# Kernel tuning notes

Hardware: AMD Instinct MI355X
Metric: run time of the kernel (lower is better)

The kernel has to match this reference:

```python
import jax, jax.numpy as jnp
import numpy as np

NUM_CONST = 20
NUM_HIDDEN = 5
NUM_VAR = 3
NUM_GROUPS = 200
INPUT_SIZE = NUM_CONST + NUM_VAR * NUM_GROUPS   # 620
HIDDEN = NUM_HIDDEN * NUM_GROUPS                # 1000
SEQ = 8192


def setup_inputs() -> dict:
    key = jax.random.key(0)
    ks = jax.random.split(key, 5)
    s = 1.0 / np.sqrt(HIDDEN)  # PyTorch LSTM init range
    return {
        "input": jax.random.normal(ks[0], (1, SEQ, INPUT_SIZE), jnp.float32),
        "W_ih": jax.random.uniform(ks[1], (4 * HIDDEN, INPUT_SIZE), jnp.float32, -s, s),
        "W_hh": jax.random.uniform(ks[2], (4 * HIDDEN, HIDDEN), jnp.float32, -s, s),
        "b_ih": jax.random.uniform(ks[3], (4 * HIDDEN,), jnp.float32, -s, s),
        "b_hh": jax.random.uniform(ks[4], (4 * HIDDEN,), jnp.float32, -s, s),
        "keep_hidden": 1,
    }


def reference(input, W_ih, W_hh, b_ih, b_hh, keep_hidden):
    # Single-layer batch_first LSTM, batch=1, zero initial (h, c) (self.hx=None).
    x = input[0]                                  # (T, I)
    # Precompute input projections for all timesteps as one big GEMM.
    xg = x @ W_ih.T + (b_ih + b_hh)               # (T, 4H)

    def step(carry, g_x):
        h, c = carry
        g = g_x + h @ W_hh.T                      # (4H,)
        i, f, gc, o = jnp.split(g, 4)             # PyTorch gate order: i, f, g, o
        i = jax.nn.sigmoid(i)
        f = jax.nn.sigmoid(f)
        gc = jnp.tanh(gc)
        o = jax.nn.sigmoid(o)
        c = f * c + i * gc
        h = o * jnp.tanh(c)
        return (h, c), h

    h0 = jnp.zeros((HIDDEN,), input.dtype)
    c0 = jnp.zeros((HIDDEN,), input.dtype)
    _, ys = jax.lax.scan(step, (h0, c0), xg)      # ys: (T, H)
    return ys[None]                               # (1, T, H)
```

## Files before the change

kernel.cpp:

```cpp
#include <hip/hip_runtime.h>
#include <hip/hip_bf16.h>


#define IN_SZ   620
#define HID     1000
#define G4      4000
#define NWF     125
#define NW_LEG  50
#define EP_LEG  20

__device__ __forceinline__ float sigm(float v)      { return 1.0f / (1.0f + __expf(-v)); }
__device__ __forceinline__ float tanh_fast(float v) { return 2.0f / (1.0f + __expf(-2.0f * v)) - 1.0f; }

__device__ __forceinline__ void stxg_(float* p, float v) { *p = v; }
__device__ __forceinline__ void stxg_(__hip_bfloat16* p, float v) { *p = __float2bfloat16(v); }

template <typename XG>
__global__ __launch_bounds__(256) void xg_gemm2(
    const float* __restrict__ x,
    const float* __restrict__ Wih,
    const float* __restrict__ bih,
    const float* __restrict__ bhh,
    XG* __restrict__ xg,
    int T)
{
    constexpr int BM = 128, BN = 128, BK = 16, LDT = BM + 4;
    __shared__ float As[BK][LDT];
    __shared__ float Bs[BK][LDT];
    const int tid = threadIdx.x;
    const int tx = tid & 15, ty = tid >> 4;
    const int m0 = blockIdx.y * BM, n0 = blockIdx.x * BN;
    float acc[8][8] = {};

    for (int k0 = 0; k0 < IN_SZ; k0 += BK) {
        #pragma unroll
        for (int it = 0; it < 2; ++it) {
            const int r = (tid >> 2) + it * 64;
            const int c = (tid & 3) * 4;
            const int gk = k0 + c;
            {
                const int gm = m0 + r;
                float4 v = {0.f, 0.f, 0.f, 0.f};
                if (gm < T) {
                    if (gk + 3 < IN_SZ) {
                        v = *reinterpret_cast<const float4*>(x + (size_t)gm * IN_SZ + gk);
                    } else {
                        const float* row = x + (size_t)gm * IN_SZ;
                        v.x = (gk + 0 < IN_SZ) ? row[gk + 0] : 0.f;
                        v.y = (gk + 1 < IN_SZ) ? row[gk + 1] : 0.f;
                        v.z = (gk + 2 < IN_SZ) ? row[gk + 2] : 0.f;
                        v.w = (gk + 3 < IN_SZ) ? row[gk + 3] : 0.f;
                    }
                }
                As[c + 0][r] = v.x; As[c + 1][r] = v.y;
                As[c + 2][r] = v.z; As[c + 3][r] = v.w;
            }
            {
                const int gn = n0 + r;
                float4 v = {0.f, 0.f, 0.f, 0.f};
                if (gn < G4) {
                    if (gk + 3 < IN_SZ) {
                        v = *reinterpret_cast<const float4*>(Wih + (size_t)gn * IN_SZ + gk);
                    } else {
                        const float* row = Wih + (size_t)gn * IN_SZ;
                        v.x = (gk + 0 < IN_SZ) ? row[gk + 0] : 0.f;
                        v.y = (gk + 1 < IN_SZ) ? row[gk + 1] : 0.f;
                        v.z = (gk + 2 < IN_SZ) ? row[gk + 2] : 0.f;
                        v.w = (gk + 3 < IN_SZ) ? row[gk + 3] : 0.f;
                    }
                }
                Bs[c + 0][r] = v.x; Bs[c + 1][r] = v.y;
                Bs[c + 2][r] = v.z; Bs[c + 3][r] = v.w;
            }
        }
        __syncthreads();
        #pragma unroll
        for (int k = 0; k < BK; ++k) {
            float a[8], b[8];
            *reinterpret_cast<float4*>(&a[0]) = *reinterpret_cast<const float4*>(&As[k][ty * 8]);
            *reinterpret_cast<float4*>(&a[4]) = *reinterpret_cast<const float4*>(&As[k][ty * 8 + 4]);
            *reinterpret_cast<float4*>(&b[0]) = *reinterpret_cast<const float4*>(&Bs[k][tx * 8]);
            *reinterpret_cast<float4*>(&b[4]) = *reinterpret_cast<const float4*>(&Bs[k][tx * 8 + 4]);
            #pragma unroll
            for (int i = 0; i < 8; ++i)
                #pragma unroll
                for (int j = 0; j < 8; ++j)
                    acc[i][j] = fmaf(a[i], b[j], acc[i][j]);
        }
        __syncthreads();
    }

    float bias[8];
    #pragma unroll
    for (int j = 0; j < 8; ++j) {
        const int n = n0 + tx * 8 + j;
        bias[j] = (n < G4) ? (bih[n] + bhh[n]) : 0.f;
    }
    #pragma unroll
    for (int i = 0; i < 8; ++i) {
        const int m = m0 + ty * 8 + i;
        if (m >= T) continue;
        #pragma unroll
        for (int j = 0; j < 8; ++j) {
            const int n = n0 + tx * 8 + j;
            if (n < G4) {
                const int g = n / 1000, e = n - g * 1000;
                stxg_(&xg[(size_t)m * G4 + e * 4 + g], acc[i][j] + bias[j]);
            }
        }
    }
}

template <int MODE>
__device__ __forceinline__ float ldxg(const void* xg_v, size_t idx) {
    if (MODE == 0) return ((const float*)xg_v)[idx];
    return __bfloat162float(((const __hip_bfloat16*)xg_v)[idx]);
}

template <int MODE>
__global__ __launch_bounds__(256, 1) void lstm_fast(
    const void* __restrict__ xg_v,
    const float* __restrict__ Whh,
    float* __restrict__ out,
    unsigned* hb_u,
    int T)
{
    __shared__ __align__(16) unsigned hs[2][1024];
    __shared__ float gsum[4][4][2];

    const int w = blockIdx.x, tid = threadIdx.x;
    const int wave = tid >> 6, lane = tid & 63;
    const int i16 = lane & 15, p = lane >> 4;
    const int we0 = w * 8 + wave * 2;

    for (int i = tid; i < 2048; i += 256) ((unsigned*)hs)[i] = 0u;
    __syncthreads();

    const size_t rowA = (size_t)(p * HID + we0) * HID;
    const size_t rowB = rowA + HID;
    float4 wA[16], wB[16], hreg[16];
    #pragma unroll
    for (int m = 0; m < 15; ++m) {
        wA[m] = *reinterpret_cast<const float4*>(Whh + rowA + i16 * 4 + m * 64);
        wB[m] = *reinterpret_cast<const float4*>(Whh + rowB + i16 * 4 + m * 64);
    }
    if (i16 < 10) {
        wA[15] = *reinterpret_cast<const float4*>(Whh + rowA + 960 + i16 * 4);
        wB[15] = *reinterpret_cast<const float4*>(Whh + rowB + 960 + i16 * 4);
    } else {
        wA[15] = float4{0.f, 0.f, 0.f, 0.f};
        wB[15] = float4{0.f, 0.f, 0.f, 0.f};
    }

    const int gv_ = (lane >> 3) & 3;
    const int gp  = (lane >> 1) & 3;
    const int ge  = lane & 1;
    const int eg  = w * 8 + gv_ * 2 + ge;
    const int xoff = (gv_ * 2 + ge) * 4 + gp;
    const int shbase = (lane & ~7) | ge;
    float c_reg = 0.0f;
    float xv = 0.0f;
    if (wave == 0 && lane < 32)
        xv = ldxg<MODE>(xg_v, (size_t)w * 32 + xoff);

    const int tid2 = tid - 64;
    const int iA = tid2;
    const int iB = (tid2 < 58) ? (192 + tid2) : tid2;

    for (int t = 0;;) {
        const int rb = t & 1;

        #pragma unroll
        for (int m = 0; m < 15; ++m)
            hreg[m] = *reinterpret_cast<const float4*>(&hs[rb][i16 * 4 + m * 64]);
        hreg[15] = *reinterpret_cast<const float4*>(&hs[rb][960 + i16 * 4]);

        float a0 = 0.f, a1 = 0.f, a2 = 0.f, a3 = 0.f;
        float b0 = 0.f, b1 = 0.f, b2 = 0.f, b3 = 0.f;
        #pragma unroll
        for (int m = 0; m < 16; ++m) {
            const float4 hv = hreg[m];
            const float sA = fmaf(wA[m].x, hv.x, fmaf(wA[m].y, hv.y,
                             fmaf(wA[m].z, hv.z, wA[m].w * hv.w)));
            const float sB = fmaf(wB[m].x, hv.x, fmaf(wB[m].y, hv.y,
                             fmaf(wB[m].z, hv.z, wB[m].w * hv.w)));
            if ((m & 3) == 0)      { a0 += sA; b0 += sB; }
            else if ((m & 3) == 1) { a1 += sA; b1 += sB; }
            else if ((m & 3) == 2) { a2 += sA; b2 += sB; }
            else                   { a3 += sA; b3 += sB; }
        }
        float rA = (a0 + a1) + (a2 + a3);
        float rB = (b0 + b1) + (b2 + b3);
        rA += __shfl_xor(rA, 1); rB += __shfl_xor(rB, 1);
        rA += __shfl_xor(rA, 2); rB += __shfl_xor(rB, 2);
        rA += __shfl_xor(rA, 4); rB += __shfl_xor(rB, 4);
        rA += __shfl_xor(rA, 8); rB += __shfl_xor(rB, 8);
        if (i16 == 0) { gsum[wave][p][0] = rA; gsum[wave][p][1] = rB; }
        __syncthreads();

        if (wave == 0) {
            float xv_next = 0.0f;
            if (lane < 32 && t + 1 < T)
                xv_next = ldxg<MODE>(xg_v, (size_t)(t + 1) * G4 + w * 32 + xoff);

            const float g = gsum[gv_][gp][ge] + xv;
            const float act = (gp == 2) ? tanh_fast(g) : sigm(g);
            const float iv = __shfl(act, shbase);
            const float fv = __shfl(act, shbase + 2);
            const float g2 = __shfl(act, shbase + 4);
            const float ov = __shfl(act, shbase + 6);
            if (lane < 32 && gp == 0) {
                c_reg = fv * c_reg + iv * g2;
                const float h = ov * tanh_fast(c_reg);
                const unsigned hb = (__float_as_uint(h) & ~3u) | (unsigned)((t + 1) & 3);
                __hip_atomic_store(hb_u + rb * 1024 + eg, hb,
                                   __ATOMIC_RELAXED, __HIP_MEMORY_SCOPE_AGENT);
                out[(size_t)t * HID + eg] = h;
            }
            xv = xv_next;
        }

        if (++t >= T) break;

        if (wave > 0) {
            const unsigned want = (unsigned)t & 3u;
            const uint4* srcb =
                reinterpret_cast<const uint4*>(hb_u + ((t - 1) & 1) * 1024);
            __builtin_amdgcn_s_sleep(8);
            uint4 vA, vB;
            for (;;) {
                asm volatile("global_load_dwordx4 %0, %2, off sc0 sc1\n\t"
                             "global_load_dwordx4 %1, %3, off sc0 sc1\n\t"
                             "s_waitcnt vmcnt(0)"
                             : "=&v"(vA), "=&v"(vB)
                             : "v"(srcb + iA), "v"(srcb + iB)
                             : "memory");
                const unsigned bad =
                    ((vA.x ^ want) | (vA.y ^ want) | (vA.z ^ want) | (vA.w ^ want) |
                     (vB.x ^ want) | (vB.y ^ want) | (vB.z ^ want) | (vB.w ^ want)) & 3u;
                if (bad == 0u) break;
            }
            uint4* dst = reinterpret_cast<uint4*>(&hs[t & 1][0]);
            dst[iA] = vA;
            if (tid2 < 58) dst[iB] = vB;
        }
        __syncthreads();
    }
}

__global__ __launch_bounds__(256, 1) void lstm_seq_legacy(
    const float* __restrict__ x,
    const float* __restrict__ Wih,
    const float* __restrict__ Whh,
    const float* __restrict__ bih,
    const float* __restrict__ bhh,
    float* __restrict__ out,
    float* hbuf, unsigned* flags, int T)
{
    __shared__ __align__(16) float h_s[HID];
    __shared__ __align__(16) float x_s[IN_SZ + 4];
    __shared__ float pre[4][EP_LEG];

    const int w = blockIdx.x, tid = threadIdx.x;
    const int wave = tid >> 6, lane = tid & 63;
    const int i16 = lane & 15, p = lane >> 4;
    const int e0 = w * EP_LEG;

    for (int i = tid; i < HID; i += 256) h_s[i] = 0.0f;
    for (int i = tid; i < IN_SZ; i += 256) x_s[i] = x[i];
    __syncthreads();

    const float* wb_h = Whh + ((size_t)wave * HID + e0) * HID;
    const float* wb_x = Wih + ((size_t)wave * HID + e0) * IN_SZ;
    float c_reg = 0.0f;
    float bsum[4] = {0.f, 0.f, 0.f, 0.f};
    if (wave == 0 && lane < EP_LEG) {
        #pragma unroll
        for (int g = 0; g < 4; ++g) {
            int n = g * HID + e0 + lane;
            bsum[g] = bih[n] + bhh[n];
        }
    }

    for (int t = 0;;) {
        #pragma unroll
        for (int pass = 0; pass < EP_LEG / 4; ++pass) {
            const int e = pass * 4 + p;
            const float* wr = wb_h + (size_t)e * HID;
            float a0 = 0.f, a1 = 0.f, a2 = 0.f, a3 = 0.f;
            #pragma unroll
            for (int m = 0; m < 15; ++m) {
                const int kk = i16 * 4 + m * 64;
                const float4 wv = *reinterpret_cast<const float4*>(wr + kk);
                const float4 hv = *reinterpret_cast<const float4*>(&h_s[kk]);
                const float s = fmaf(wv.x, hv.x, fmaf(wv.y, hv.y, fmaf(wv.z, hv.z, wv.w * hv.w)));
                if ((m & 3) == 0) a0 += s; else if ((m & 3) == 1) a1 += s;
                else if ((m & 3) == 2) a2 += s; else a3 += s;
            }
            if (i16 < 10) {
                const int kk = i16 * 4 + 960;
                const float4 wv = *reinterpret_cast<const float4*>(wr + kk);
                const float4 hv = *reinterpret_cast<const float4*>(&h_s[kk]);
                a3 += fmaf(wv.x, hv.x, fmaf(wv.y, hv.y, fmaf(wv.z, hv.z, wv.w * hv.w)));
            }
            const float* wrx = wb_x + (size_t)e * IN_SZ;
            #pragma unroll
            for (int m = 0; m < 9; ++m) {
                const int kk = i16 * 4 + m * 64;
                const float4 wv = *reinterpret_cast<const float4*>(wrx + kk);
                const float4 hv = *reinterpret_cast<const float4*>(&x_s[kk]);
                const float s = fmaf(wv.x, hv.x, fmaf(wv.y, hv.y, fmaf(wv.z, hv.z, wv.w * hv.w)));
                if ((m & 3) == 0) a0 += s; else if ((m & 3) == 1) a1 += s;
                else if ((m & 3) == 2) a2 += s; else a3 += s;
            }
            if (i16 < 11) {
                const int kk = i16 * 4 + 576;
                const float4 wv = *reinterpret_cast<const float4*>(wrx + kk);
                const float4 hv = *reinterpret_cast<const float4*>(&x_s[kk]);
                a3 += fmaf(wv.x, hv.x, fmaf(wv.y, hv.y, fmaf(wv.z, hv.z, wv.w * hv.w)));
            }
            float acc = (a0 + a1) + (a2 + a3);
            acc += __shfl_xor(acc, 1);
            acc += __shfl_xor(acc, 2);
            acc += __shfl_xor(acc, 4);
            acc += __shfl_xor(acc, 8);
            if (i16 == 0) pre[wave][e] = acc;
        }
        __syncthreads();

        if (wave == 0 && lane < EP_LEG) {
            const float gi = pre[0][lane] + bsum[0];
            const float gf = pre[1][lane] + bsum[1];
            const float gg = pre[2][lane] + bsum[2];
            const float go = pre[3][lane] + bsum[3];
            const float iv = sigm(gi);
            const float fv = sigm(gf);
            const float gv = tanh_fast(gg);
            const float ov = sigm(go);
            c_reg = fv * c_reg + iv * gv;
            const float h = ov * tanh_fast(c_reg);
            out[(size_t)t * HID + e0 + lane] = h;
            __hip_atomic_store(&hbuf[(t & 1) * 1024 + e0 + lane], h,
                               __ATOMIC_RELAXED, __HIP_MEMORY_SCOPE_AGENT);
        }
        if (++t >= T) break;
        if (wave == 0 && lane == 0) {
            asm volatile("s_waitcnt vmcnt(0)" ::: "memory");
            __hip_atomic_store(&flags[w], (unsigned)t,
                               __ATOMIC_RELAXED, __HIP_MEMORY_SCOPE_AGENT);
        }
        if (wave > 0) {
            if (lane < NW_LEG) {
                while (__hip_atomic_load(&flags[lane], __ATOMIC_RELAXED,
                                         __HIP_MEMORY_SCOPE_AGENT) < (unsigned)t) {}
            }
            const int rb = tid - 64;
            for (int i = rb; i < HID; i += 192) {
                h_s[i] = __hip_atomic_load(&hbuf[((t - 1) & 1) * 1024 + i],
                                           __ATOMIC_RELAXED, __HIP_MEMORY_SCOPE_AGENT);
            }
            for (int i = rb; i < IN_SZ; i += 192) x_s[i] = x[(size_t)t * IN_SZ + i];
        }
        __syncthreads();
    }
}

extern "C" void kernel_launch(void* const* d_in, const int* in_sizes, int n_in,
                              void* d_out, int out_size, void* d_ws, size_t ws_size,
                              hipStream_t stream)
{
    const float* x   = (const float*)d_in[0];
    const float* Wih = (const float*)d_in[1];
    const float* Whh = (const float*)d_in[2];
    const float* bih = (const float*)d_in[3];
    const float* bhh = (const float*)d_in[4];
    float* out = (float*)d_out;
    const int T = in_sizes[0] / IN_SZ;

    char* ws = (char*)d_ws;
    unsigned* hb_u  = (unsigned*)ws;
    unsigned* flags = (unsigned*)(ws + 8192);
    const size_t CTRL = 16384;
    (void)hipMemsetAsync(d_ws, 0, CTRL, stream);

    const size_t need32 = CTRL + (size_t)T * G4 * sizeof(float);
    const size_t need16 = CTRL + (size_t)T * G4 * sizeof(__hip_bfloat16);

    dim3 g1((G4 + 127) / 128, (T + 127) / 128), b1(256);

    if (ws_size >= need32) {
        float* xgbuf = (float*)(ws + CTRL);
        xg_gemm2<float><<<g1, b1, 0, stream>>>(x, Wih, bih, bhh, xgbuf, T);
        lstm_fast<0><<<dim3(NWF), dim3(256), 0, stream>>>(xgbuf, Whh, out, hb_u, T);
    } else if (ws_size >= need16) {
        __hip_bfloat16* xgbuf = (__hip_bfloat16*)(ws + CTRL);
        xg_gemm2<__hip_bfloat16><<<g1, b1, 0, stream>>>(x, Wih, bih, bhh, xgbuf, T);
        lstm_fast<1><<<dim3(NWF), dim3(256), 0, stream>>>(xgbuf, Whh, out, hb_u, T);
    } else {
        lstm_seq_legacy<<<dim3(NW_LEG), dim3(256), 0, stream>>>(
            x, Wih, Whh, bih, bhh, out, (float*)hb_u, flags, T);
    }
}
```

Before: 19.28 ms.

## Split recurrent LSTM across 250 workgroups with one hidden unit per wave

Doubles the persistent recurrent kernel's workgroup count so each wave holds the W_hh rows for one hidden unit instead of two. This halves per-wave register weight storage and per-step FMA work, and shrinks the gate reduction and shuffle. It relies on 250 co-resident workgroups on the device and raises the number of participants in the per-step cross-workgroup h exchange. The xg layout and index mapping change to match.

```diff
diff --git a/kernel.cpp b/kernel.cpp
--- a/kernel.cpp
+++ b/kernel.cpp
@@ -5,7 +5,7 @@
 #define IN_SZ   620
 #define HID     1000
 #define G4      4000
-#define NWF     125
+#define NWF     250
 #define NW_LEG  50
 #define EP_LEG  20
 
@@ -126,42 +126,34 @@
     int T)
 {
     __shared__ __align__(16) unsigned hs[2][1024];
-    __shared__ float gsum[4][4][2];
+    __shared__ float gsum[4][4];
 
     const int w = blockIdx.x, tid = threadIdx.x;
     const int wave = tid >> 6, lane = tid & 63;
     const int i16 = lane & 15, p = lane >> 4;
-    const int we0 = w * 8 + wave * 2;
+    const int hi = w * 4 + wave;
 
     for (int i = tid; i < 2048; i += 256) ((unsigned*)hs)[i] = 0u;
     __syncthreads();
 
-    const size_t rowA = (size_t)(p * HID + we0) * HID;
-    const size_t rowB = rowA + HID;
-    float4 wA[16], wB[16], hreg[16];
+    const size_t rowA = (size_t)(p * HID + hi) * HID;
+    float4 wA[16], hreg[16];
     #pragma unroll
-    for (int m = 0; m < 15; ++m) {
+    for (int m = 0; m < 15; ++m)
         wA[m] = *reinterpret_cast<const float4*>(Whh + rowA + i16 * 4 + m * 64);
-        wB[m] = *reinterpret_cast<const float4*>(Whh + rowB + i16 * 4 + m * 64);
-    }
-    if (i16 < 10) {
-        wA[15] = *reinterpret_cast<const float4*>(Whh + rowA + 960 + i16 * 4);
-        wB[15] = *reinterpret_cast<const float4*>(Whh + rowB + 960 + i16 * 4);
-    } else {
-        wA[15] = float4{0.f, 0.f, 0.f, 0.f};
-        wB[15] = float4{0.f, 0.f, 0.f, 0.f};
-    }
-
-    const int gv_ = (lane >> 3) & 3;
-    const int gp  = (lane >> 1) & 3;
-    const int ge  = lane & 1;
-    const int eg  = w * 8 + gv_ * 2 + ge;
-    const int xoff = (gv_ * 2 + ge) * 4 + gp;
-    const int shbase = (lane & ~7) | ge;
+    wA[15] = (i16 < 10)
+        ? *reinterpret_cast<const float4*>(Whh + rowA + 960 + i16 * 4)
+        : float4{0.f, 0.f, 0.f, 0.f};
+
+    const int ge_ = lane >> 2;
+    const int gp  = lane & 3;
+    const int eg  = w * 4 + ge_;
+    const int xoff = lane;
+    const int shbase = lane & ~3;
     float c_reg = 0.0f;
     float xv = 0.0f;
-    if (wave == 0 && lane < 32)
-        xv = ldxg<MODE>(xg_v, (size_t)w * 32 + xoff);
+    if (wave == 0 && lane < 16)
+        xv = ldxg<MODE>(xg_v, (size_t)w * 16 + xoff);
 
     const int tid2 = tid - 64;
     const int iA = tid2;
@@ -176,40 +168,36 @@
         hreg[15] = *reinterpret_cast<const float4*>(&hs[rb][960 + i16 * 4]);
 
         float a0 = 0.f, a1 = 0.f, a2 = 0.f, a3 = 0.f;
-        float b0 = 0.f, b1 = 0.f, b2 = 0.f, b3 = 0.f;
         #pragma unroll
         for (int m = 0; m < 16; ++m) {
             const float4 hv = hreg[m];
             const float sA = fmaf(wA[m].x, hv.x, fmaf(wA[m].y, hv.y,
                              fmaf(wA[m].z, hv.z, wA[m].w * hv.w)));
-            const float sB = fmaf(wB[m].x, hv.x, fmaf(wB[m].y, hv.y,
-                             fmaf(wB[m].z, hv.z, wB[m].w * hv.w)));
-            if ((m & 3) == 0)      { a0 += sA; b0 += sB; }
-            else if ((m & 3) == 1) { a1 += sA; b1 += sB; }
-            else if ((m & 3) == 2) { a2 += sA; b2 += sB; }
-            else                   { a3 += sA; b3 += sB; }
+            if ((m & 3) == 0)      a0 += sA;
+            else if ((m & 3) == 1) a1 += sA;
+            else if ((m & 3) == 2) a2 += sA;
+            else                   a3 += sA;
         }
         float rA = (a0 + a1) + (a2 + a3);
-        float rB = (b0 + b1) + (b2 + b3);
-        rA += __shfl_xor(rA, 1); rB += __shfl_xor(rB, 1);
-        rA += __shfl_xor(rA, 2); rB += __shfl_xor(rB, 2);
-        rA += __shfl_xor(rA, 4); rB += __shfl_xor(rB, 4);
-        rA += __shfl_xor(rA, 8); rB += __shfl_xor(rB, 8);
-        if (i16 == 0) { gsum[wave][p][0] = rA; gsum[wave][p][1] = rB; }
+        rA += __shfl_xor(rA, 1);
+        rA += __shfl_xor(rA, 2);
+        rA += __shfl_xor(rA, 4);
+        rA += __shfl_xor(rA, 8);
+        if (i16 == 0) gsum[wave][p] = rA;
         __syncthreads();
 
         if (wave == 0) {
             float xv_next = 0.0f;
-            if (lane < 32 && t + 1 < T)
-                xv_next = ldxg<MODE>(xg_v, (size_t)(t + 1) * G4 + w * 32 + xoff);
-
-            const float g = gsum[gv_][gp][ge] + xv;
+            if (lane < 16 && t + 1 < T)
+                xv_next = ldxg<MODE>(xg_v, (size_t)(t + 1) * G4 + w * 16 + xoff);
+
+            const float g = gsum[ge_][gp] + xv;
             const float act = (gp == 2) ? tanh_fast(g) : sigm(g);
-            const float iv = __shfl(act, shbase);
-            const float fv = __shfl(act, shbase + 2);
-            const float g2 = __shfl(act, shbase + 4);
-            const float ov = __shfl(act, shbase + 6);
-            if (lane < 32 && gp == 0) {
+            const float iv = __shfl(act, shbase + 0);
+            const float fv = __shfl(act, shbase + 1);
+            const float g2 = __shfl(act, shbase + 2);
+            const float ov = __shfl(act, shbase + 3);
+            if (lane < 16 && gp == 0) {
                 c_reg = fv * c_reg + iv * g2;
                 const float h = ov * tanh_fast(c_reg);
                 const unsigned hb = (__float_as_uint(h) & ~3u) | (unsigned)((t + 1) & 3);
```

After: 23.49 ms. 1.22x slower.
